# Kernel optimization log

Measured on AMD Instinct MI355X. Metric: run time of the kernel, lower is better.

## Reference

```python
import jax, jax.numpy as jnp
import numpy as np

WS = 7          # window size
SHIFT = WS // 2 # shift for odd blocks
NH = 8          # num heads
EPS = 1e-5


def _rel_pos_index(ws):
    coords = np.stack(np.meshgrid(np.arange(ws), np.arange(ws), indexing='ij'))  # (2, ws, ws)
    cf = coords.reshape(2, -1)                                  # (2, N)
    rc = (cf[:, :, None] - cf[:, None, :]).transpose(1, 2, 0)   # (N, N, 2)
    rc[..., 0] += ws - 1
    rc[..., 1] += ws - 1
    rc[..., 0] *= 2 * ws - 1
    return rc.sum(-1)  # (N, N) int


def _attn_mask(Hp, Wp, ws, shift):
    # (nW, N, N) additive mask with 0 / -100, as in the torch code
    img = np.zeros((Hp, Wp), dtype=np.float32)
    cnt = 0
    slices = (slice(0, -ws), slice(-ws, -shift), slice(-shift, None))
    for h in slices:
        for w in slices:
            img[h, w] = cnt
            cnt += 1
    mw = img.reshape(Hp // ws, ws, Wp // ws, ws).transpose(0, 2, 1, 3).reshape(-1, ws * ws)
    am = mw[:, None, :] - mw[:, :, None]
    return np.where(am != 0, -100.0, 0.0).astype(np.float32)


def _layernorm(x, w, b):
    m = x.mean(-1, keepdims=True)
    v = ((x - m) ** 2).mean(-1, keepdims=True)
    return (x - m) * jax.lax.rsqrt(v + EPS) * w + b


def _window_partition(x, ws):
    B, H, W, C = x.shape
    x = x.reshape(B, H // ws, ws, W // ws, ws, C).transpose(0, 1, 3, 2, 4, 5)
    return x.reshape(-1, ws * ws, C)


def _window_reverse(w, ws, H, W):
    B = w.shape[0] // (H // ws * W // ws)
    x = w.reshape(B, H // ws, W // ws, ws, ws, -1).transpose(0, 1, 3, 2, 4, 5)
    return x.reshape(B, H, W, -1)


def _window_msa(xw, qkv_w, qkv_b, proj_w, proj_b, rpb, rel_idx, mask):
    Bw, N, C = xw.shape
    hd = C // NH
    qkv = (xw @ qkv_w.T + qkv_b).reshape(Bw, N, 3, NH, hd).transpose(2, 0, 3, 1, 4)
    q, k, v = qkv[0] * (hd ** -0.5), qkv[1], qkv[2]
    attn = jnp.einsum('bhnd,bhmd->bhnm', q, k)                      # (Bw, NH, N, N)
    bias = rpb[rel_idx.reshape(-1)].reshape(N, N, NH).transpose(2, 0, 1)
    attn = attn + bias[None]
    if mask is not None:
        nW = mask.shape[0]
        attn = attn.reshape(Bw // nW, nW, NH, N, N) + mask[None, :, None]
        attn = attn.reshape(Bw, NH, N, N)
    attn = jax.nn.softmax(attn, axis=-1)
    out = jnp.einsum('bhnm,bhmd->bhnd', attn, v).transpose(0, 2, 1, 3).reshape(Bw, N, C)
    return out @ proj_w.T + proj_b


def _forward(x, ln1_w, ln1_b, qkv_w, qkv_b, proj_w, proj_b, rpb,
             ln2_w, ln2_b, mlp_w1, mlp_b1, mlp_w2, mlp_b2, H, W):
    B, L, C = x.shape
    rel_idx = _rel_pos_index(WS)
    pad_r = (WS - W % WS) % WS
    pad_b = (WS - H % WS) % WS
    Hp, Wp = H + pad_b, W + pad_r
    depth = ln1_w.shape[0]
    for i in range(depth):
        shift = 0 if i % 2 == 0 else SHIFT
        shortcut = x
        h = _layernorm(x, ln1_w[i], ln1_b[i]).reshape(B, H, W, C)
        if pad_r > 0 or pad_b > 0:
            h = jnp.pad(h, ((0, 0), (0, pad_b), (0, pad_r), (0, 0)))
        if shift > 0:
            h = jnp.roll(h, (-shift, -shift), axis=(1, 2))
            mask = jnp.asarray(_attn_mask(Hp, Wp, WS, shift))
        else:
            mask = None
        hw = _window_partition(h, WS)
        hw = _window_msa(hw, qkv_w[i], qkv_b[i], proj_w[i], proj_b[i], rpb[i], rel_idx, mask)
        h = _window_reverse(hw.reshape(-1, WS, WS, C), WS, Hp, Wp)
        if shift > 0:
            h = jnp.roll(h, (shift, shift), axis=(1, 2))
        if pad_r > 0 or pad_b > 0:
            h = h[:, :H, :W, :]
        x = shortcut + h.reshape(B, H * W, C)
        m = _layernorm(x, ln2_w[i], ln2_b[i])
        m = jax.nn.gelu(m @ mlp_w1[i].T + mlp_b1[i], approximate=False)
        x = x + (m @ mlp_w2[i].T + mlp_b2[i])
    return x


def setup_inputs() -> dict:
    key = jax.random.key(0)
    ks = jax.random.split(key, 8)
    B, H, W, C, D = 8, 112, 112, 256, 2
    hid = 4 * C
    return {
        'x': jax.random.normal(ks[0], (B, H * W, C), jnp.float32),
        'ln1_w': jnp.ones((D, C), jnp.float32),
        'ln1_b': jnp.zeros((D, C), jnp.float32),
        'qkv_w': jax.random.normal(ks[1], (D, 3 * C, C), jnp.float32) * 0.02,
        'qkv_b': jnp.zeros((D, 3 * C), jnp.float32),
        'proj_w': jax.random.normal(ks[2], (D, C, C), jnp.float32) * 0.02,
        'proj_b': jnp.zeros((D, C), jnp.float32),
        'rpb': jax.random.normal(ks[3], (D, (2 * WS - 1) ** 2, NH), jnp.float32) * 0.02,
        'ln2_w': jnp.ones((D, C), jnp.float32),
        'ln2_b': jnp.zeros((D, C), jnp.float32),
        'mlp_w1': jax.random.normal(ks[4], (D, hid, C), jnp.float32) * 0.02,
        'mlp_b1': jnp.zeros((D, hid), jnp.float32),
        'mlp_w2': jax.random.normal(ks[5], (D, C, hid), jnp.float32) * 0.02,
        'mlp_b2': jnp.zeros((D, C), jnp.float32),
        'H': H,
        'W': W,
    }


def reference(x, ln1_w, ln1_b, qkv_w, qkv_b, proj_w, proj_b, rpb,
              ln2_w, ln2_b, mlp_w1, mlp_b1, mlp_w2, mlp_b2, H, W):
    return _forward(x, ln1_w, ln1_b, qkv_w, qkv_b, proj_w, proj_b, rpb,
                    ln2_w, ln2_b, mlp_w1, mlp_b1, mlp_w2, mlp_b2, H, W)
```

## Files before the change

kernel.cpp:

```cpp
#include <hip/hip_runtime.h>

typedef unsigned short u16;
typedef unsigned int u32;
typedef __attribute__((ext_vector_type(8))) short bf16x8;
typedef __attribute__((ext_vector_type(4))) float f32x4;
typedef __attribute__((ext_vector_type(16))) float f32x16;
typedef __attribute__((ext_vector_type(8))) unsigned short u16x8;
typedef const __attribute__((address_space(1))) void gvoid;
typedef __attribute__((address_space(3))) void svoid;

#define T_TOK 100352
#define CDIM 256
#define ATTN_SCALE 0.17677669529663687f

__device__ __forceinline__ u16 f2bf(float f) {
    u32 u = __float_as_uint(f);
    u32 r = (u + 0x7fffu + ((u >> 16) & 1u)) >> 16;
    return (u16)r;
}
__device__ __forceinline__ float bf2f(u16 h) {
    return __uint_as_float(((u32)h) << 16);
}
__device__ __forceinline__ float gelu_f(float x) {
    return 0.5f * x * (1.0f + erff(x * 0.70710678118654752f));
}
__device__ __forceinline__ int div7(int q) { return (q * 37) >> 8; }
__device__ __forceinline__ int reg3(int r) { return r < 105 ? 0 : (r < 109 ? 1 : 2); }

__global__ void cvt_kernel(const float* __restrict__ in, u16* __restrict__ out, int n) {
    int i = blockIdx.x * 256 + threadIdx.x;
    if (i < n) out[i] = f2bf(in[i]);
}

__global__ __launch_bounds__(256) void ln_kernel(
    const float* __restrict__ X, const float* __restrict__ w,
    const float* __restrict__ b, u16* __restrict__ Y)
{
    int wid = threadIdx.x >> 6, l = threadIdx.x & 63;
    int t = blockIdx.x * 4 + wid;
    const float4 x4 = ((const float4*)(X + (size_t)t * CDIM))[l];
    float s  = x4.x + x4.y + x4.z + x4.w;
    float s2 = x4.x*x4.x + x4.y*x4.y + x4.z*x4.z + x4.w*x4.w;
    #pragma unroll
    for (int o = 32; o; o >>= 1) { s += __shfl_xor(s, o); s2 += __shfl_xor(s2, o); }
    float mean = s * (1.0f/256.0f);
    float var  = s2 * (1.0f/256.0f) - mean*mean;
    float rstd = rsqrtf(var + 1e-5f);
    float4 w4 = ((const float4*)w)[l];
    float4 b4 = ((const float4*)b)[l];
    ushort4 o4;
    o4.x = f2bf((x4.x - mean)*rstd*w4.x + b4.x);
    o4.y = f2bf((x4.y - mean)*rstd*w4.y + b4.y);
    o4.z = f2bf((x4.z - mean)*rstd*w4.z + b4.z);
    o4.w = f2bf((x4.w - mean)*rstd*w4.w + b4.w);
    ((ushort4*)(Y + (size_t)t * CDIM))[l] = o4;
}

template<int EPI>
__global__ __launch_bounds__(256) void gemm_kernel(
    const u16* __restrict__ A, const u16* __restrict__ Bw,
    const float* __restrict__ bias, void* __restrict__ outp,
    const float* __restrict__ res, int N, int K, int nTn)
{
    __shared__ __align__(16) u16 lds[2][2][128 * 64];
    const int tid = threadIdx.x;
    const int l = tid & 63;
    const int w = tid >> 6;
    const int wr = w >> 1, wc = w & 1;

    const int nBlocks = gridDim.x;
    const int cpx = nBlocks >> 3;
    const int lin = (blockIdx.x & 7) * cpx + (blockIdx.x >> 3);
    const int nT = lin % nTn;
    const int mT = lin / nTn;

    f32x4 acc[4][4];
    #pragma unroll
    for (int m = 0; m < 4; ++m)
        #pragma unroll
        for (int n = 0; n < 4; ++n) acc[m][n] = (f32x4){0.f,0.f,0.f,0.f};

    const int sr = tid >> 3;
    const int sg = tid & 7;

    #define STAGE(buf, kt)                                                              \
        {                                                                               \
            _Pragma("unroll")                                                           \
            for (int c = 0; c < 4; ++c) {                                               \
                int r = c*32 + sr;                                                      \
                int gsrc = sg ^ (r & 7);                                                \
                const u16* ga = A  + (size_t)(mT*128 + r) * K + (kt) + gsrc*8;          \
                const u16* gb = Bw + (size_t)(nT*128 + r) * K + (kt) + gsrc*8;          \
                u16* la = &lds[buf][0][(c*256 + w*64) * 8];                              \
                u16* lb = &lds[buf][1][(c*256 + w*64) * 8];                              \
                __builtin_amdgcn_global_load_lds((gvoid*)ga, (svoid*)la, 16, 0, 0);     \
                __builtin_amdgcn_global_load_lds((gvoid*)gb, (svoid*)lb, 16, 0, 0);     \
            }                                                                           \
        }

    const int nSteps = K >> 6;
    int cur = 0;

    STAGE(0, 0);
    asm volatile("s_waitcnt vmcnt(0)" ::: "memory");
    __builtin_amdgcn_s_barrier();
    asm volatile("" ::: "memory");

    const int lr = l & 15, gq = l >> 4;
    for (int t = 0; t < nSteps; ++t) {
        bf16x8 a[2][4], b[2][4];
        #pragma unroll
        for (int kk = 0; kk < 2; ++kk) {
            #pragma unroll
            for (int m = 0; m < 4; ++m) {
                int r = wr*64 + m*16 + lr;
                int g = kk*4 + gq;
                a[kk][m] = *(const bf16x8*)&lds[cur][0][r*64 + (g ^ (r & 7))*8];
            }
            #pragma unroll
            for (int n = 0; n < 4; ++n) {
                int r = wc*64 + n*16 + lr;
                int g = kk*4 + gq;
                b[kk][n] = *(const bf16x8*)&lds[cur][1][r*64 + (g ^ (r & 7))*8];
            }
        }
        if (t + 1 < nSteps) STAGE(cur ^ 1, (t + 1) * 64);

        __builtin_amdgcn_s_setprio(1);
        #pragma unroll
        for (int kk = 0; kk < 2; ++kk)
            #pragma unroll
            for (int m = 0; m < 4; ++m)
                #pragma unroll
                for (int n = 0; n < 4; ++n)
                    acc[m][n] = __builtin_amdgcn_mfma_f32_16x16x32_bf16(a[kk][m], b[kk][n], acc[m][n], 0, 0, 0);
        __builtin_amdgcn_s_setprio(0);

        asm volatile("s_waitcnt vmcnt(0)" ::: "memory");
        __builtin_amdgcn_s_barrier();
        asm volatile("" ::: "memory");
        cur ^= 1;
    }
    #undef STAGE

    const int lr4 = gq * 4;
    const int lcn = lr;
    #pragma unroll
    for (int m = 0; m < 4; ++m) {
        #pragma unroll
        for (int n = 0; n < 4; ++n) {
            int row0 = mT*128 + wr*64 + m*16 + lr4;
            int col  = nT*128 + wc*64 + n*16 + lcn;
            float bb = bias[col];
            #pragma unroll
            for (int j = 0; j < 4; ++j) {
                size_t idx = (size_t)(row0 + j) * N + col;
                float v = acc[m][n][j] + bb;
                if (EPI == 0)      ((u16*)outp)[idx] = f2bf(v);
                else if (EPI == 1) ((u16*)outp)[idx] = f2bf(gelu_f(v));
                else               ((float*)outp)[idx] = v + res[idx];
            }
        }
    }
}

__global__ __launch_bounds__(256) void attn_kernel(
    const u16* __restrict__ qkv, const float* __restrict__ rpb,
    u16* __restrict__ outb, int shift)
{
    __shared__ u16 Vt[8][2048];
    __shared__ float biasl[8 * 176];
    __shared__ int tok[64];

    const int t = threadIdx.x;
    const int w = t >> 6;
    const int l = t & 63;
    const int lo = l & 31;
    const int hi = l >> 5;
    const int win = blockIdx.x;
    const int wj = win & 15, wi = (win >> 4) & 15, bb = win >> 8;

    if (t < 64) {
        int qq = t > 48 ? 48 : t;
        int i = div7(qq), j = qq - i*7;
        int rr = wi*7 + i + shift; if (rr >= 112) rr -= 112;
        int cc = wj*7 + j + shift; if (cc >= 112) cc -= 112;
        tok[t] = bb*12544 + rr*112 + cc;
    }
    for (int i2 = t; i2 < 1352; i2 += 256)
        biasl[(i2 & 7)*176 + (i2 >> 3)] = rpb[i2];
    __syncthreads();

    int iqv[2], jqv[2], regq[2];
    #pragma unroll
    for (int nt = 0; nt < 2; ++nt) {
        int q = nt*32 + lo; int qb = q > 48 ? 48 : q;
        int iq = div7(qb), jq = qb - iq*7;
        iqv[nt] = iq; jqv[nt] = jq;
        regq[nt] = 0;
        if (shift > 0) regq[nt] = reg3(wi*7 + iq)*3 + reg3(wj*7 + jq);
    }

    #pragma unroll 1
    for (int hh = 0; hh < 2; ++hh) {
        const int h = 2*w + hh;

        {
            u16x8 vreg[4];
            if (l < 49) {
                const u16x8* vs = (const u16x8*)(qkv + (size_t)tok[l]*768 + 512 + h*32);
                #pragma unroll
                for (int c4 = 0; c4 < 4; ++c4) vreg[c4] = vs[c4];
            } else {
                #pragma unroll
                for (int c4 = 0; c4 < 4; ++c4) vreg[c4] = (u16x8){0,0,0,0,0,0,0,0};
            }
            u16* vt = &Vt[h][0];
            #pragma unroll
            for (int c4 = 0; c4 < 4; ++c4)
                #pragma unroll
                for (int e = 0; e < 8; ++e)
                    vt[(c4*8 + e)*64 + (l ^ (e << 3))] = vreg[c4][e];
        }

        bf16x8 kf[2][2], qf[2][2];
        #pragma unroll
        for (int mt = 0; mt < 2; ++mt)
            #pragma unroll
            for (int td = 0; td < 2; ++td)
                kf[mt][td] = *(const bf16x8*)(qkv + (size_t)tok[mt*32 + lo]*768 + 256 + h*32 + td*16 + hi*8);
        #pragma unroll
        for (int nt = 0; nt < 2; ++nt)
            #pragma unroll
            for (int td = 0; td < 2; ++td)
                qf[nt][td] = *(const bf16x8*)(qkv + (size_t)tok[nt*32 + lo]*768 + h*32 + td*16 + hi*8);

        f32x16 s[2][2];
        #pragma unroll
        for (int mt = 0; mt < 2; ++mt)
            #pragma unroll
            for (int nt = 0; nt < 2; ++nt) {
                f32x16 z;
                #pragma unroll
                for (int i = 0; i < 16; ++i) z[i] = 0.f;
                s[mt][nt] = z;
            }
        #pragma unroll
        for (int td = 0; td < 2; ++td)
            #pragma unroll
            for (int mt = 0; mt < 2; ++mt)
                #pragma unroll
                for (int nt = 0; nt < 2; ++nt)
                    s[mt][nt] = __builtin_amdgcn_mfma_f32_32x32x16_bf16(kf[mt][td], qf[nt][td], s[mt][nt], 0, 0, 0);

        asm volatile("s_waitcnt lgkmcnt(0)" ::: "memory");
        __builtin_amdgcn_sched_barrier(0);

        const float* bh = biasl + h*176;
        #pragma unroll
        for (int mt = 0; mt < 2; ++mt) {
            #pragma unroll
            for (int i = 0; i < 16; ++i) {
                int r = (i & 3) + 8*(i >> 2) + 4*hi;
                int k = mt*32 + r;
                bool valid = k < 49;
                int kb = valid ? k : 48;
                int ik = div7(kb), jk = kb - ik*7;
                int regk = 0;
                if (shift > 0) regk = reg3(wi*7 + ik)*3 + reg3(wj*7 + jk);
                #pragma unroll
                for (int nt = 0; nt < 2; ++nt) {
                    float v = s[mt][nt][i] * ATTN_SCALE
                            + bh[(iqv[nt] - ik + 6)*13 + (jqv[nt] - jk + 6)];
                    if (shift > 0 && regq[nt] != regk) v -= 100.0f;
                    if (!valid) v = -1e30f;
                    s[mt][nt][i] = v;
                }
            }
        }

        #pragma unroll
        for (int nt = 0; nt < 2; ++nt) {
            float mx = -1e30f;
            #pragma unroll
            for (int i = 0; i < 16; ++i) mx = fmaxf(mx, fmaxf(s[0][nt][i], s[1][nt][i]));
            mx = fmaxf(mx, __shfl_xor(mx, 32));
            float sum = 0.f;
            #pragma unroll
            for (int mt = 0; mt < 2; ++mt)
                #pragma unroll
                for (int i = 0; i < 16; ++i) {
                    float e = __expf(s[mt][nt][i] - mx);
                    s[mt][nt][i] = e;
                    sum += e;
                }
            sum += __shfl_xor(sum, 32);
            float inv = __builtin_amdgcn_rcpf(sum);

            u32 pk[2][8];
            #pragma unroll
            for (int mt = 0; mt < 2; ++mt)
                #pragma unroll
                for (int j = 0; j < 8; ++j)
                    pk[mt][j] = (u32)f2bf(s[mt][nt][2*j] * inv)
                              | ((u32)f2bf(s[mt][nt][2*j + 1] * inv) << 16);

            f32x16 o;
            #pragma unroll
            for (int i = 0; i < 16; ++i) o[i] = 0.f;
            #pragma unroll
            for (int kt = 0; kt < 4; ++kt) {
                const int mt = kt >> 1;
                const int base = (kt & 1) * 4;
                u32 a0 = pk[mt][base + 0], a1 = pk[mt][base + 1];
                u32 a2 = pk[mt][base + 2], a3 = pk[mt][base + 3];
                asm volatile("v_permlane32_swap_b32 %0, %1" : "+v"(a0), "+v"(a2));
                asm volatile("v_permlane32_swap_b32 %0, %1" : "+v"(a1), "+v"(a3));
                union { u32 u[4]; bf16x8 v; } pf;
                pf.u[0] = a0; pf.u[1] = a1; pf.u[2] = a2; pf.u[3] = a3;
                bf16x8 vb = *(const bf16x8*)(&Vt[h][lo*64 + ((kt*16 + hi*8) ^ ((lo & 7) << 3))]);
                o = __builtin_amdgcn_mfma_f32_32x32x16_bf16(pf.v, vb, o, 0, 0, 0);
            }

            #pragma unroll
            for (int i = 0; i < 16; ++i) {
                int q = nt*32 + (i & 3) + 8*(i >> 2) + 4*hi;
                if (q < 49)
                    outb[(size_t)tok[q]*256 + h*32 + lo] = f2bf(o[i]);
            }
        }
    }
}

extern "C" void kernel_launch(void* const* d_in, const int* in_sizes, int n_in,
                              void* d_out, int out_size, void* d_ws, size_t ws_size,
                              hipStream_t stream) {
    const float* x_in   = (const float*)d_in[0];
    const float* ln1_w  = (const float*)d_in[1];
    const float* ln1_b  = (const float*)d_in[2];
    const float* qkv_w  = (const float*)d_in[3];
    const float* qkv_b  = (const float*)d_in[4];
    const float* proj_w = (const float*)d_in[5];
    const float* proj_b = (const float*)d_in[6];
    const float* rpb    = (const float*)d_in[7];
    const float* ln2_w  = (const float*)d_in[8];
    const float* ln2_b  = (const float*)d_in[9];
    const float* mlp_w1 = (const float*)d_in[10];
    const float* mlp_b1 = (const float*)d_in[11];
    const float* mlp_w2 = (const float*)d_in[12];
    const float* mlp_b2 = (const float*)d_in[13];
    float* xout = (float*)d_out;

    char* p = (char*)d_ws;
    u16* wq = (u16*)p;  p += (size_t)2*768*256*2;
    u16* wp = (u16*)p;  p += (size_t)2*256*256*2;
    u16* w1 = (u16*)p;  p += (size_t)2*1024*256*2;
    u16* w2 = (u16*)p;  p += (size_t)2*256*1024*2;
    u16* buf_y   = (u16*)p; p += (size_t)T_TOK*256*2;
    u16* buf_big = (u16*)p;

    {
        int n;
        n = 2*768*256;  cvt_kernel<<<(n+255)/256, 256, 0, stream>>>(qkv_w,  wq, n);
        n = 2*256*256;  cvt_kernel<<<(n+255)/256, 256, 0, stream>>>(proj_w, wp, n);
        n = 2*1024*256; cvt_kernel<<<(n+255)/256, 256, 0, stream>>>(mlp_w1, w1, n);
        n = 2*256*1024; cvt_kernel<<<(n+255)/256, 256, 0, stream>>>(mlp_w2, w2, n);
    }

    for (int i = 0; i < 2; ++i) {
        const int shift = (i == 0) ? 0 : 3;
        const float* xcur = (i == 0) ? x_in : xout;

        ln_kernel<<<T_TOK/4, 256, 0, stream>>>(xcur, ln1_w + i*256, ln1_b + i*256, buf_y);
        gemm_kernel<0><<<784*6, 256, 0, stream>>>(
            buf_y, wq + (size_t)i*768*256, qkv_b + i*768, buf_big, nullptr, 768, 256, 6);
        attn_kernel<<<2048, 256, 0, stream>>>(buf_big, rpb + i*169*8, buf_y, shift);
        gemm_kernel<2><<<784*2, 256, 0, stream>>>(
            buf_y, wp + (size_t)i*256*256, proj_b + i*256, xout, xcur, 256, 256, 2);
        ln_kernel<<<T_TOK/4, 256, 0, stream>>>(xout, ln2_w + i*256, ln2_b + i*256, buf_y);
        gemm_kernel<1><<<784*8, 256, 0, stream>>>(
            buf_y, w1 + (size_t)i*1024*256, mlp_b1 + i*1024, buf_big, nullptr, 1024, 256, 8);
        gemm_kernel<2><<<784*2, 256, 0, stream>>>(
            buf_big, w2 + (size_t)i*256*1024, mlp_b2 + i*256, xout, xout, 256, 1024, 2);
    }
}
```

Baseline: 1.052 ms.

## Stage GEMM epilogue through LDS for vectorized stores and use tanh GELU

Result: faster. 1.001 ms (-4.8%).

```diff
diff --git a/kernel.cpp b/kernel.cpp
--- a/kernel.cpp
+++ b/kernel.cpp
@@ -22,7 +22,10 @@
     return __uint_as_float(((u32)h) << 16);
 }
 __device__ __forceinline__ float gelu_f(float x) {
-    return 0.5f * x * (1.0f + erff(x * 0.70710678118654752f));
+    float z = 0.7978845608028654f * (x + 0.044715f * x * x * x);
+    float e = __expf(2.0f * z);
+    float th = 1.0f - 2.0f * __builtin_amdgcn_rcpf(e + 1.0f);
+    return 0.5f * x * (1.0f + th);
 }
 __device__ __forceinline__ int div7(int q) { return (q * 37) >> 8; }
 __device__ __forceinline__ int reg3(int r) { return r < 105 ? 0 : (r < 109 ? 1 : 2); }
@@ -62,7 +65,8 @@
     const float* __restrict__ bias, void* __restrict__ outp,
     const float* __restrict__ res, int N, int K, int nTn)
 {
-    __shared__ __align__(16) u16 lds[2][2][128 * 64];
+    __shared__ __align__(16) char lds_raw[69632];
+    u16 (*lds)[2][128 * 64] = (u16(*)[2][128 * 64])lds_raw;
     const int tid = threadIdx.x;
     const int l = tid & 63;
     const int w = tid >> 6;
@@ -143,23 +147,51 @@
     }
     #undef STAGE
 
-    const int lr4 = gq * 4;
-    const int lcn = lr;
-    #pragma unroll
-    for (int m = 0; m < 4; ++m) {
-        #pragma unroll
-        for (int n = 0; n < 4; ++n) {
-            int row0 = mT*128 + wr*64 + m*16 + lr4;
-            int col  = nT*128 + wc*64 + n*16 + lcn;
-            float bb = bias[col];
-            #pragma unroll
-            for (int j = 0; j < 4; ++j) {
-                size_t idx = (size_t)(row0 + j) * N + col;
-                float v = acc[m][n][j] + bb;
-                if (EPI == 0)      ((u16*)outp)[idx] = f2bf(v);
-                else if (EPI == 1) ((u16*)outp)[idx] = f2bf(gelu_f(v));
-                else               ((float*)outp)[idx] = v + res[idx];
-            }
+    if (EPI == 2) {
+        float* epf = (float*)lds_raw + w * (64 * 68);
+        #pragma unroll
+        for (int m = 0; m < 4; ++m)
+            #pragma unroll
+            for (int n = 0; n < 4; ++n) {
+                float bb = bias[nT*128 + wc*64 + n*16 + lr];
+                #pragma unroll
+                for (int j = 0; j < 4; ++j)
+                    epf[(m*16 + gq*4 + j)*68 + n*16 + lr] = acc[m][n][j] + bb;
+            }
+        const int rr4 = l >> 4, cc4 = (l & 15) * 4;
+        float* outf = (float*)outp;
+        #pragma unroll
+        for (int p = 0; p < 16; ++p) {
+            float4 vv = *(const float4*)&epf[(p*4 + rr4)*68 + cc4];
+            size_t grow = (size_t)(mT*128 + wr*64 + p*4 + rr4);
+            size_t gcol = (size_t)(nT*128 + wc*64 + cc4);
+            float4 rv = *(const float4*)(res + grow*N + gcol);
+            float4 ov; ov.x = vv.x + rv.x; ov.y = vv.y + rv.y;
+            ov.z = vv.z + rv.z; ov.w = vv.w + rv.w;
+            *(float4*)(outf + grow*N + gcol) = ov;
+        }
+    } else {
+        u16* ep = (u16*)lds_raw + w * (64 * 72);
+        #pragma unroll
+        for (int m = 0; m < 4; ++m)
+            #pragma unroll
+            for (int n = 0; n < 4; ++n) {
+                float bb = bias[nT*128 + wc*64 + n*16 + lr];
+                #pragma unroll
+                for (int j = 0; j < 4; ++j) {
+                    float v = acc[m][n][j] + bb;
+                    if (EPI == 1) v = gelu_f(v);
+                    ep[(m*16 + gq*4 + j)*72 + n*16 + lr] = f2bf(v);
+                }
+            }
+        const int rr8 = l >> 3, cc8 = (l & 7) * 8;
+        u16* outw = (u16*)outp;
+        #pragma unroll
+        for (int p = 0; p < 8; ++p) {
+            u16x8 vv = *(const u16x8*)&ep[(p*8 + rr8)*72 + cc8];
+            size_t grow = (size_t)(mT*128 + wr*64 + p*8 + rr8);
+            size_t gcol = (size_t)(nT*128 + wc*64 + cc8);
+            *(u16x8*)(outw + grow*N + gcol) = vv;
         }
     }
 }
```
